# Optimization experiments

Hardware: AMD Instinct MI355X
Metric: run time of the kernel (lower is better)

## Reference

```python
import jax, jax.numpy as jnp
import numpy as np

B, D, H, Q, N, V = 2048, 2048, 16, 128, 8192, 128


def setup_inputs() -> dict:
    key = jax.random.key(0)
    k1, k2, k3, k4, k5 = jax.random.split(key, 5)
    return {
        "x": jax.random.normal(k1, (B, D), dtype=jnp.float32),
        "keys": jax.random.normal(k2, (N, Q), dtype=jnp.float32),
        "values": jax.random.normal(k3, (N, V), dtype=jnp.float32),
        "Wq": jax.random.normal(k4, (H * Q, D), dtype=jnp.float32) * (1.0 / np.sqrt(D)),
        "Wo": jax.random.normal(k5, (D, H * V), dtype=jnp.float32) * (1.0 / np.sqrt(H * V)),
    }


def reference(x, keys, values, Wq, Wo):
    b = x.shape[0]
    h, q = H, Q
    # queries: [B, H, Q]
    queries = (x @ Wq.T).reshape(b, h, q)
    # einsum 'aib,ajb->aijb' then sum over last axis == dot product over Q
    scores = jnp.einsum('bhq,nq->bhn', queries, keys) / jnp.sqrt(jnp.asarray(q, x.dtype))
    attn = jax.nn.softmax(scores, axis=-1)  # [B, H, N]
    # Original: einsum('aib,ajc->aijc', attn, values) sums attn over its N axis
    # (label b) independently of values' N axis (label j), giving
    # out[a,i,j,c] = attn_rowsum[a,i] * values[j,c]; mean over j then yields
    # attn_rowsum[a,i] * mean_n(values)[c]. Computed here without the [B,H,N,V]
    # intermediate (mathematically identical).
    attn_rowsum = attn.sum(axis=-1)        # [B, H] (== 1 up to fp error)
    vmean = values.mean(axis=0)            # [V]
    outv = (attn_rowsum[:, :, None] * vmean[None, None, :]).reshape(b, -1)  # [B, H*V]
    return outv @ Wo.T + x
```

## Files before the change

### kernel.cpp

```cpp
#include <hip/hip_runtime.h>


#define NROWS 8192
#define VDIM  128
#define DDIM  2048
#define BDIM  2048
#define VBLK  256
#define WBLK  768

__global__ void __launch_bounds__(256) prep_kernel(
    const float4* __restrict__ vals4,
    const float4* __restrict__ Wo4,
    float4* __restrict__ partial4,
    float4* __restrict__ WoF4)
{
    __shared__ float4 s[256];
    const int t = threadIdx.x;
    const int bid = blockIdx.x;

    if (bid < VBLK) {
        float4 acc = make_float4(0.f, 0.f, 0.f, 0.f);
        const int base = bid * 1024;
#pragma unroll
        for (int j = 0; j < 4; ++j) {
            float4 v = vals4[base + t + 256 * j];
            acc.x += v.x; acc.y += v.y; acc.z += v.z; acc.w += v.w;
        }
        s[t] = acc;
        __syncthreads();
        if (t < 32) {
            float4 r = s[t];
#pragma unroll
            for (int k = 1; k < 8; ++k) {
                float4 v = s[t + 32 * k];
                r.x += v.x; r.y += v.y; r.z += v.z; r.w += v.w;
            }
            partial4[bid * 32 + t] = r;
        }
    } else {
        const int wb = bid - VBLK;
        const int vq = t & 31;
        const int hg = t >> 5;
        for (int d = wb; d < DDIM; d += WBLK) {
            const float4* row = Wo4 + (size_t)d * 512;
            float4 a = row[(2 * hg) * 32 + vq];
            float4 b = row[(2 * hg + 1) * 32 + vq];
            a.x += b.x; a.y += b.y; a.z += b.z; a.w += b.w;
            s[t] = a;
            __syncthreads();
            if (t < 32) {
                float4 r = s[t];
#pragma unroll
                for (int k = 1; k < 8; ++k) {
                    float4 v = s[t + 32 * k];
                    r.x += v.x; r.y += v.y; r.z += v.z; r.w += v.w;
                }
                WoF4[d * 32 + t] = r;
            }
            __syncthreads();
        }
    }
}

__global__ void __launch_bounds__(256) c_kernel(
    const float4* __restrict__ partial4,
    const float4* __restrict__ WoF4,
    float* __restrict__ cvec)
{
    __shared__ float4 s[256];
    __shared__ float4 vm_lds[32];
    const int t = threadIdx.x;

    float4 acc = make_float4(0.f, 0.f, 0.f, 0.f);
#pragma unroll
    for (int j = 0; j < 32; ++j) {
        float4 v = partial4[t + 256 * j];
        acc.x += v.x; acc.y += v.y; acc.z += v.z; acc.w += v.w;
    }
    s[t] = acc;
    __syncthreads();
    if (t < 32) {
        float4 r = s[t];
#pragma unroll
        for (int k = 1; k < 8; ++k) {
            float4 v = s[t + 32 * k];
            r.x += v.x; r.y += v.y; r.z += v.z; r.w += v.w;
        }
        const float inv = 1.0f / (float)NROWS;
        r.x *= inv; r.y *= inv; r.z *= inv; r.w *= inv;
        vm_lds[t] = r;
    }
    __syncthreads();

    const int dl = t >> 2;
    const int part = t & 3;
    const int d = blockIdx.x * 64 + dl;
    float dot = 0.f;
#pragma unroll
    for (int j = 0; j < 8; ++j) {
        float4 w = WoF4[(size_t)d * 32 + part * 8 + j];
        float4 vm = vm_lds[part * 8 + j];
        dot += w.x * vm.x + w.y * vm.y + w.z * vm.z + w.w * vm.w;
    }
    dot += __shfl_xor(dot, 1);
    dot += __shfl_xor(dot, 2);
    if (part == 0) cvec[d] = dot;
}

__global__ void __launch_bounds__(256) add_kernel(
    const float4* __restrict__ x4,
    const float* __restrict__ cvec,
    float4* __restrict__ out4)
{
    const float4* __restrict__ c4 = (const float4*)cvec;
    const int t = threadIdx.x;
    const size_t base = (size_t)blockIdx.x * 512 + t;
    float4 xv0 = x4[base];
    float4 xv1 = x4[base + 256];
    float4 cv0 = c4[t];
    float4 cv1 = c4[t + 256];
    xv0.x += cv0.x; xv0.y += cv0.y; xv0.z += cv0.z; xv0.w += cv0.w;
    xv1.x += cv1.x; xv1.y += cv1.y; xv1.z += cv1.z; xv1.w += cv1.w;
    out4[base] = xv0;
    out4[base + 256] = xv1;
}

extern "C" void kernel_launch(void* const* d_in, const int* in_sizes, int n_in,
                              void* d_out, int out_size, void* d_ws, size_t ws_size,
                              hipStream_t stream) {
    const float* x      = (const float*)d_in[0];
    const float* values = (const float*)d_in[2];
    const float* Wo     = (const float*)d_in[4];
    float* out = (float*)d_out;
    float* ws  = (float*)d_ws;

    float4* partial4 = (float4*)ws;
    float4* WoF4     = (float4*)(ws + 32768);
    float*  cvec     = ws + 32768 + 262144;

    prep_kernel<<<VBLK + WBLK, 256, 0, stream>>>((const float4*)values,
                                                 (const float4*)Wo,
                                                 partial4, WoF4);
    c_kernel<<<32, 256, 0, stream>>>(partial4, WoF4, cvec);
    add_kernel<<<2048, 256, 0, stream>>>((const float4*)x, cvec, (float4*)out);
}
```

Baseline: 20.56 us.

## Fold Wo head-sum into c_kernel and shrink values column-sum grid

The values column-sum now runs on its own in 64 blocks, each reading 16 rows-worth of float4s instead of 4. The Wo head-folding is moved out of the prep kernel into c_kernel: 512 blocks each load 4 rows of Wo directly, fold the heads and dot with the mean vector in registers, and reduce through LDS and shuffles. This removes the intermediate WoF buffer write and read and the serialized loop in the prep kernel. In exchange, every one of the 512 c_kernel blocks redundantly re-reduces the 2048 partial vectors to get the mean.

After: 19.92 us (median of 2 runs). -3.1%, faster.

```diff
diff --git a/kernel.cpp b/kernel.cpp
--- a/kernel.cpp
+++ b/kernel.cpp
@@ -5,75 +5,55 @@
 #define VDIM  128
 #define DDIM  2048
 #define BDIM  2048
-#define VBLK  256
-#define WBLK  768
 
-__global__ void __launch_bounds__(256) prep_kernel(
+__global__ void __launch_bounds__(256) colsum_kernel(
     const float4* __restrict__ vals4,
-    const float4* __restrict__ Wo4,
-    float4* __restrict__ partial4,
-    float4* __restrict__ WoF4)
+    float4* __restrict__ partial4)
 {
     __shared__ float4 s[256];
     const int t = threadIdx.x;
     const int bid = blockIdx.x;
-
-    if (bid < VBLK) {
-        float4 acc = make_float4(0.f, 0.f, 0.f, 0.f);
-        const int base = bid * 1024;
+    float4 acc = make_float4(0.f, 0.f, 0.f, 0.f);
+    const int base = bid * 4096;
 #pragma unroll
-        for (int j = 0; j < 4; ++j) {
-            float4 v = vals4[base + t + 256 * j];
-            acc.x += v.x; acc.y += v.y; acc.z += v.z; acc.w += v.w;
+    for (int j = 0; j < 16; ++j) {
+        float4 v = vals4[base + t + 256 * j];
+        acc.x += v.x; acc.y += v.y; acc.z += v.z; acc.w += v.w;
+    }
+    s[t] = acc;
+    __syncthreads();
+    if (t < 32) {
+        float4 r = s[t];
+#pragma unroll
+        for (int k = 1; k < 8; ++k) {
+            float4 v = s[t + 32 * k];
+            r.x += v.x; r.y += v.y; r.z += v.z; r.w += v.w;
         }
-        s[t] = acc;
-        __syncthreads();
-        if (t < 32) {
-            float4 r = s[t];
-#pragma unroll
-            for (int k = 1; k < 8; ++k) {
-                float4 v = s[t + 32 * k];
-                r.x += v.x; r.y += v.y; r.z += v.z; r.w += v.w;
-            }
-            partial4[bid * 32 + t] = r;
-        }
-    } else {
-        const int wb = bid - VBLK;
-        const int vq = t & 31;
-        const int hg = t >> 5;
-        for (int d = wb; d < DDIM; d += WBLK) {
-            const float4* row = Wo4 + (size_t)d * 512;
-            float4 a = row[(2 * hg) * 32 + vq];
-            float4 b = row[(2 * hg + 1) * 32 + vq];
-            a.x += b.x; a.y += b.y; a.z += b.z; a.w += b.w;
-            s[t] = a;
-            __syncthreads();
-            if (t < 32) {
-                float4 r = s[t];
-#pragma unroll
-                for (int k = 1; k < 8; ++k) {
-                    float4 v = s[t + 32 * k];
-                    r.x += v.x; r.y += v.y; r.z += v.z; r.w += v.w;
-                }
-                WoF4[d * 32 + t] = r;
-            }
-            __syncthreads();
-        }
+        partial4[bid * 32 + t] = r;
     }
 }
 
 __global__ void __launch_bounds__(256) c_kernel(
     const float4* __restrict__ partial4,
-    const float4* __restrict__ WoF4,
-    float* __restrict__ cvec)
+    const float4* __restrict__ Wo4,
+    float4* __restrict__ cvec4)
 {
     __shared__ float4 s[256];
     __shared__ float4 vm_lds[32];
     const int t = threadIdx.x;
+    const int d0 = blockIdx.x * 4;
+
+    float4 w[4][2];
+#pragma unroll
+    for (int r = 0; r < 4; ++r) {
+        const float4* row = Wo4 + (size_t)(d0 + r) * 512;
+        w[r][0] = row[t];
+        w[r][1] = row[t + 256];
+    }
 
     float4 acc = make_float4(0.f, 0.f, 0.f, 0.f);
 #pragma unroll
-    for (int j = 0; j < 32; ++j) {
+    for (int j = 0; j < 8; ++j) {
         float4 v = partial4[t + 256 * j];
         acc.x += v.x; acc.y += v.y; acc.z += v.z; acc.w += v.w;
     }
@@ -92,19 +72,36 @@
     }
     __syncthreads();
 
-    const int dl = t >> 2;
-    const int part = t & 3;
-    const int d = blockIdx.x * 64 + dl;
-    float dot = 0.f;
+    const float4 vm = vm_lds[t & 31];
+    float4 dots;
+    {
+        float* dp = (float*)&dots;
 #pragma unroll
-    for (int j = 0; j < 8; ++j) {
-        float4 w = WoF4[(size_t)d * 32 + part * 8 + j];
-        float4 vm = vm_lds[part * 8 + j];
-        dot += w.x * vm.x + w.y * vm.y + w.z * vm.z + w.w * vm.w;
+        for (int r = 0; r < 4; ++r) {
+            float4 a = w[r][0], b = w[r][1];
+            a.x += b.x; a.y += b.y; a.z += b.z; a.w += b.w;
+            dp[r] = a.x * vm.x + a.y * vm.y + a.z * vm.z + a.w * vm.w;
+        }
     }
-    dot += __shfl_xor(dot, 1);
-    dot += __shfl_xor(dot, 2);
-    if (part == 0) cvec[d] = dot;
+    s[t] = dots;
+    __syncthreads();
+
+    if (t < 64) {
+        float4 r = s[t];
+#pragma unroll
+        for (int k = 1; k < 4; ++k) {
+            float4 v = s[t + 64 * k];
+            r.x += v.x; r.y += v.y; r.z += v.z; r.w += v.w;
+        }
+#pragma unroll
+        for (int off = 32; off; off >>= 1) {
+            r.x += __shfl_down(r.x, off);
+            r.y += __shfl_down(r.y, off);
+            r.z += __shfl_down(r.z, off);
+            r.w += __shfl_down(r.w, off);
+        }
+        if (t == 0) cvec4[blockIdx.x] = r;
+    }
 }
 
 __global__ void __launch_bounds__(256) add_kernel(
@@ -128,19 +125,16 @@
 extern "C" void kernel_launch(void* const* d_in, const int* in_sizes, int n_in,
                               void* d_out, int out_size, void* d_ws, size_t ws_size,
                               hipStream_t stream) {
-    const float* x      = (const float*)d_in[0];
-    const float* values = (const float*)d_in[2];
-    const float* Wo     = (const float*)d_in[4];
-    float* out = (float*)d_out;
-    float* ws  = (float*)d_ws;
+    const float4* vals4 = (const float4*)d_in[2];
+    const float4* Wo4   = (const float4*)d_in[4];
+    const float4* x4    = (const float4*)d_in[0];
+    float4* out4 = (float4*)d_out;
+    char* ws = (char*)d_ws;
 
     float4* partial4 = (float4*)ws;
-    float4* WoF4     = (float4*)(ws + 32768);
-    float*  cvec     = ws + 32768 + 262144;
+    float4* cvec4    = (float4*)(ws + 32768);
 
-    prep_kernel<<<VBLK + WBLK, 256, 0, stream>>>((const float4*)values,
-                                                 (const float4*)Wo,
-                                                 partial4, WoF4);
-    c_kernel<<<32, 256, 0, stream>>>(partial4, WoF4, cvec);
-    add_kernel<<<2048, 256, 0, stream>>>((const float4*)x, cvec, (float4*)out);
+    colsum_kernel<<<64, 256, 0, stream>>>(vals4, partial4);
+    c_kernel<<<512, 256, 0, stream>>>(partial4, Wo4, cvec4);
+    add_kernel<<<2048, 256, 0, stream>>>(x4, (const float*)cvec4, out4);
 }
```
